# Kernel tuning notes

Measured on AMD Instinct MI355X. Metric: run time of the kernel, lower is better.

The kernel has to match this reference:

```python
import jax, jax.numpy as jnp
import numpy as np

DIM = 256          # model dim
H = 8              # num heads
E = DIM // H       # head dim = 32
M = 32             # ball size
NB = 8192          # number of balls
N = NB * M         # total points = 262144
D3 = 3             # spatial dimensionality


def setup_inputs() -> dict:
    key = jax.random.key(0)
    ks = jax.random.split(key, 10)
    s = 1.0 / np.sqrt(DIM)
    return {
        "x": jax.random.normal(ks[0], (N, DIM), jnp.float32),
        "pos": jax.random.normal(ks[1], (N, D3), jnp.float32),
        "w_qkv": jax.random.normal(ks[2], (DIM, 3 * DIM), jnp.float32) * s,
        "b_qkv": jnp.zeros((3 * DIM,), jnp.float32),
        "w_pe": jax.random.normal(ks[3], (D3, DIM), jnp.float32) * (1.0 / np.sqrt(D3)),
        "b_pe": jnp.zeros((DIM,), jnp.float32),
        "w_proj": jax.random.normal(ks[4], (DIM, DIM), jnp.float32) * s,
        "b_proj": jnp.zeros((DIM,), jnp.float32),
        "sigma_att": -1.0 + 0.01 * jax.random.normal(ks[5], (1, H, 1, 1), jnp.float32),
    }


def reference(x, pos, w_qkv, b_qkv, w_pe, b_pe, w_proj, b_proj, sigma_att):
    n = x.shape[0] // M
    pos_b = pos.reshape(n, M, D3)                       # (n, m, 3)

    # eq. 9: relative position embedding wrt ball center
    centers = pos_b.mean(axis=1, keepdims=True)         # (n, 1, 3)
    rel = (pos_b - centers).reshape(n * M, D3)
    x = x + rel @ w_pe + b_pe                           # (N, DIM)

    # qkv projection; layout '(H E K)' with K fastest
    qkv = (x @ w_qkv + b_qkv).reshape(n, M, H, E, 3)
    q = jnp.transpose(qkv[..., 0], (0, 2, 1, 3))        # (n, H, m, E)
    k = jnp.transpose(qkv[..., 1], (0, 2, 1, 3))
    v = jnp.transpose(qkv[..., 2], (0, 2, 1, 3))

    # eq. 10: distance-based attention bias
    diff = pos_b[:, :, None, :] - pos_b[:, None, :, :]  # (n, m, m, 3)
    d2 = jnp.sum(diff * diff, axis=-1)
    dist = jnp.sqrt(jnp.maximum(d2, 1e-12))             # safe sqrt (grad at 0)
    bias = sigma_att * dist[:, None, :, :]              # (n, H, m, m)

    scale = 1.0 / np.sqrt(E)
    scores = jnp.einsum('nhme,nhke->nhmk', q, k) * scale + bias
    attn = jax.nn.softmax(scores, axis=-1)
    out = jnp.einsum('nhmk,nhke->nhme', attn, v)        # (n, H, m, E)
    out = jnp.transpose(out, (0, 2, 1, 3)).reshape(n * M, DIM)
    return out @ w_proj + b_proj
```

## Files before the change

### kernel.cpp

```cpp
#include <hip/hip_runtime.h>

#define NPTS   262144
#define NBALLS 8192
#define MSZ    32

typedef unsigned short u16;
typedef __attribute__((ext_vector_type(8))) unsigned short u16x8;
typedef __attribute__((ext_vector_type(4))) unsigned short u16x4;
typedef __attribute__((ext_vector_type(8))) __bf16 bf16x8;
typedef __attribute__((ext_vector_type(4))) float f32x4;
typedef __attribute__((ext_vector_type(2))) unsigned u32x2;

__device__ inline u16 f2bf(float f) {
    unsigned u = __builtin_bit_cast(unsigned, f);
    u += 0x7fffu + ((u >> 16) & 1u);
    return (u16)(u >> 16);
}

__device__ inline unsigned pk2(float lo, float hi) {
    return (unsigned)f2bf(lo) | ((unsigned)f2bf(hi) << 16);
}

__device__ inline f32x4 mfma16(u16x8 a, u16x8 b, f32x4 c) {
    return __builtin_amdgcn_mfma_f32_16x16x32_bf16(
        __builtin_bit_cast(bf16x8, a), __builtin_bit_cast(bf16x8, b), c, 0, 0, 0);
}

__device__ inline void gload_lds16(const u16* g, u16* l) {
    __builtin_amdgcn_global_load_lds(
        (const __attribute__((address_space(1))) void*)g,
        (__attribute__((address_space(3))) void*)l, 16, 0, 0);
}

__global__ __launch_bounds__(256) void k0_wprep(const float* __restrict__ w_qkv,
                                                const float* __restrict__ b_qkv,
                                                const float* __restrict__ w_proj,
                                                u16* __restrict__ wqkvT,
                                                u16* __restrict__ wpF,
                                                float* __restrict__ bq) {
    int idx = blockIdx.x * 256 + threadIdx.x;
    if (idx < 768 * 256) {
        int cp = idx >> 8, r = idx & 255;
        int k = cp >> 8, rem = cp & 255, h = rem >> 5, e = rem & 31;
        int orig = h * 96 + e * 3 + k;
        wqkvT[cp * 256 + r] = f2bf(w_qkv[r * 768 + orig]);
        if (r == 0) bq[cp] = b_qkv[orig];
    } else {
        int tid2 = idx - 768 * 256;
        int lane = tid2 & 63, ch = tid2 >> 6;
        int hk = ch & 7, gct = ch >> 3;
        int r15 = lane & 15, g4 = lane >> 4;
        u16x8 o;
#pragma unroll
        for (int j = 0; j < 8; ++j)
            o[j] = f2bf(w_proj[(size_t)(hk * 32 + g4 * 8 + j) * 256 + gct * 16 + r15]);
        *(u16x8*)&wpF[(size_t)tid2 * 8] = o;
    }
}

__global__ __launch_bounds__(512, 4) void k1_qkv(const float* __restrict__ x,
                                                 const float* __restrict__ pos,
                                                 const float* __restrict__ w_pe,
                                                 const float* __restrict__ b_pe,
                                                 const u16* __restrict__ wqkvT,
                                                 const float* __restrict__ bq,
                                                 u16* __restrict__ qkv2) {
    __shared__ __align__(16) u16 Astage[128 * 64];
    __shared__ __align__(16) u16 Bs[2][128 * 64];
    __shared__ float ps_s[384];
    __shared__ float ctr_s[4][3];
    __shared__ float rel_s[128][3];
    __shared__ float wpe_s[3][256];
    __shared__ float bpe_s[256];

    int id = blockIdx.x;
    int rt = (id >> 3) + (id & 7) * 256;
    int t = threadIdx.x;
    int lane = t & 63, wv = t >> 6;
    int r15 = lane & 15, g4 = lane >> 4;
    int wr = wv >> 1, wc = wv & 1;
    int rowbase = rt * 128;

    if (t < 384) ps_s[t] = pos[(size_t)rt * 384 + t];
    if (t < 256) bpe_s[t] = b_pe[t];
    for (int i = t; i < 768; i += 512) ((float*)wpe_s)[i] = w_pe[i];
    __syncthreads();
    if (t < 12) {
        int b = t / 3, m = t % 3;
        float s = 0.f;
#pragma unroll
        for (int j = 0; j < MSZ; ++j) s += ps_s[(b * 32 + j) * 3 + m];
        ctr_s[b][m] = s * (1.0f / MSZ);
    }
    __syncthreads();
    if (t < 384) {
        int p = t / 3, m = t % 3;
        ((float*)rel_s)[t] = ps_s[t] - ctr_s[p >> 5][m];
    }
#pragma unroll
    for (int i = 0; i < 2; ++i) {
        int c = i * 512 + t;
        int row = c >> 3, sg = c & 7;
        gload_lds16(&wqkvT[(size_t)row * 256 + (sg ^ (row & 7)) * 8], &Bs[0][c * 8]);
    }
    __syncthreads();

    u16x8 af[2][8];
#pragma unroll
    for (int kt = 0; kt < 4; ++kt) {
#pragma unroll
        for (int i = 0; i < 2; ++i) {
            int c = i * 512 + t;
            int row = c >> 3, g = c & 7;
            int kk0 = kt * 64 + g * 8;
            float4 xa = *(const float4*)&x[(size_t)(rowbase + row) * 256 + kk0];
            float4 xb = *(const float4*)&x[(size_t)(rowbase + row) * 256 + kk0 + 4];
            float r0 = rel_s[row][0], r1 = rel_s[row][1], r2 = rel_s[row][2];
            u16x8 o;
#pragma unroll
            for (int m = 0; m < 8; ++m) {
                float xv = (m < 4) ? ((const float*)&xa)[m] : ((const float*)&xb)[m - 4];
                float v = fmaf(r0, wpe_s[0][kk0 + m],
                          fmaf(r1, wpe_s[1][kk0 + m],
                          fmaf(r2, wpe_s[2][kk0 + m], xv))) + bpe_s[kk0 + m];
                o[m] = f2bf(v);
            }
            *(u16x8*)&Astage[(row * 8 + (g ^ (row & 7))) * 8] = o;
        }
        __syncthreads();
#pragma unroll
        for (int ks = 0; ks < 2; ++ks)
#pragma unroll
            for (int i = 0; i < 2; ++i) {
                int R = wr * 32 + i * 16 + r15;
                af[i][2 * kt + ks] =
                    *(const u16x8*)&Astage[R * 64 + (((ks * 4 + g4) ^ (R & 7)) * 8)];
            }
        __syncthreads();
    }

    f32x4 acc[4][2];
#pragma unroll
    for (int j = 0; j < 4; ++j)
#pragma unroll
        for (int i = 0; i < 2; ++i) acc[j][i] = (f32x4){0.f, 0.f, 0.f, 0.f};

    const int ball = rt * 4 + wr;
    for (int ct = 0; ct < 6; ++ct) {
#pragma unroll
        for (int kt = 0; kt < 4; ++kt) {
            int cur = kt & 1;
            if (kt < 3 || ct < 5) {
                int nct = (kt < 3) ? ct : ct + 1;
                int nkt = (kt < 3) ? kt + 1 : 0;
#pragma unroll
                for (int i = 0; i < 2; ++i) {
                    int c = i * 512 + t;
                    int row = c >> 3, sg = c & 7;
                    gload_lds16(&wqkvT[(size_t)(nct * 128 + row) * 256 + nkt * 64 + (sg ^ (row & 7)) * 8],
                                &Bs[cur ^ 1][c * 8]);
                }
            }
#pragma unroll
            for (int ks = 0; ks < 2; ++ks) {
                u16x8 b[4];
#pragma unroll
                for (int j = 0; j < 4; ++j) {
                    int C = wc * 64 + j * 16 + r15;
                    b[j] = *(const u16x8*)&Bs[cur][C * 64 + (((ks * 4 + g4) ^ (C & 7)) * 8)];
                }
#pragma unroll
                for (int j = 0; j < 4; ++j)
#pragma unroll
                    for (int i = 0; i < 2; ++i)
                        acc[j][i] = mfma16(b[j], af[i][2 * kt + ks], acc[j][i]);
            }
            if (kt == 3) {
#pragma unroll
                for (int j = 0; j < 4; ++j) {
                    int cp0 = ct * 128 + wc * 64 + j * 16 + g4 * 4;
                    float4 bias = *(const float4*)&bq[cp0];
                    int mat = cp0 >> 8, rem = cp0 & 255, h = rem >> 5, e0 = rem & 31;
                    size_t base = (size_t)ball * 24576 + mat * 8192 + h * 1024 + e0;
#pragma unroll
                    for (int i = 0; i < 2; ++i) {
                        int point = i * 16 + r15;
                        unsigned lo = pk2(acc[j][i][0] + bias.x, acc[j][i][1] + bias.y);
                        unsigned hi = pk2(acc[j][i][2] + bias.z, acc[j][i][3] + bias.w);
                        *(u32x2*)&qkv2[base + point * 32] = (u32x2){lo, hi};
                        acc[j][i] = (f32x4){0.f, 0.f, 0.f, 0.f};
                    }
                }
            }
            __syncthreads();
        }
    }
}

__global__ __launch_bounds__(256) void k23_attnproj(const float* __restrict__ pos,
                                                    const float* __restrict__ sigma,
                                                    const u16* __restrict__ qkv2,
                                                    const u16* __restrict__ wpF,
                                                    const float* __restrict__ bp,
                                                    float* __restrict__ out) {
    int ball = blockIdx.x, t = threadIdx.x;
    __shared__ float ps[MSZ][3];
    __shared__ float dist_s[MSZ][33];
    __shared__ __align__(16) u16 V_s[MSZ][256];
    __shared__ __align__(16) u16 P_s[4][MSZ][40];
    __shared__ __align__(16) u16 ao_s[MSZ][264];

    const size_t ballbase = (size_t)ball * 24576;

    if (t < MSZ * 3) ((float*)ps)[t] = pos[(size_t)ball * (MSZ * 3) + t];
    __syncthreads();
    for (int p = t; p < 1024; p += 256) {
        int m = p >> 5, k = p & 31;
        float dx = ps[m][0] - ps[k][0], dy = ps[m][1] - ps[k][1], dz = ps[m][2] - ps[k][2];
        dist_s[m][k] = sqrtf(fmaxf(dx * dx + dy * dy + dz * dz, 1e-12f));
    }
#pragma unroll
    for (int i = 0; i < 4; ++i) {
        int c = i * 256 + t;
        int h = c >> 7, wi = c & 127;
        int point = wi >> 2, g4w = wi & 3;
        int col8 = h * 32 + g4w * 8;
        int cs = col8 ^ (((point >> 3) & 3) << 4);
        *(u16x8*)&V_s[point][cs] = *(const u16x8*)&qkv2[ballbase + 16384 + (size_t)c * 8];
    }
    __syncthreads();

    int lane = t & 63, wv = t >> 6;
    int r15 = lane & 15, g4 = lane >> 4;
    const float scale = 0.17677669529663687f;

#pragma unroll
    for (int hh = 0; hh < 2; ++hh) {
        int h = wv * 2 + hh;
        float sig = sigma[h];
        u16x8 aq[2], bk[2];
#pragma unroll
        for (int i = 0; i < 2; ++i) {
            aq[i] = *(const u16x8*)&qkv2[ballbase + h * 1024 + (size_t)(i * 16 + r15) * 32 + g4 * 8];
            bk[i] = *(const u16x8*)&qkv2[ballbase + 8192 + h * 1024 + (size_t)(i * 16 + r15) * 32 + g4 * 8];
        }
        f32x4 s[2][2];
#pragma unroll
        for (int i = 0; i < 2; ++i)
#pragma unroll
            for (int j = 0; j < 2; ++j) s[i][j] = (f32x4){0.f, 0.f, 0.f, 0.f};
#pragma unroll
        for (int i = 0; i < 2; ++i)
#pragma unroll
            for (int j = 0; j < 2; ++j)
                s[i][j] = mfma16(aq[i], bk[j], s[i][j]);

#pragma unroll
        for (int i = 0; i < 2; ++i) {
#pragma unroll
            for (int r = 0; r < 4; ++r) {
                int row = i * 16 + g4 * 4 + r;
                float v0 = s[i][0][r] * scale + sig * dist_s[row][r15];
                float v1 = s[i][1][r] * scale + sig * dist_s[row][16 + r15];
                float m = fmaxf(v0, v1);
                m = fmaxf(m, __shfl_xor(m, 1));
                m = fmaxf(m, __shfl_xor(m, 2));
                m = fmaxf(m, __shfl_xor(m, 4));
                m = fmaxf(m, __shfl_xor(m, 8));
                float e0 = __expf(v0 - m), e1 = __expf(v1 - m);
                float su = e0 + e1;
                su += __shfl_xor(su, 1);
                su += __shfl_xor(su, 2);
                su += __shfl_xor(su, 4);
                su += __shfl_xor(su, 8);
                float rin = 1.0f / su;
                P_s[wv][row][r15]      = f2bf(e0 * rin);
                P_s[wv][row][16 + r15] = f2bf(e1 * rin);
            }
        }
        u16x8 pa[2];
#pragma unroll
        for (int i = 0; i < 2; ++i)
            pa[i] = *(const u16x8*)&P_s[wv][i * 16 + r15][g4 * 8];
        u16x8 bv[2];
#pragma unroll
        for (int j = 0; j < 2; ++j) {
#pragma unroll
            for (int jj = 0; jj < 8; ++jj) {
                int kp = g4 * 8 + jj;
                int colv = h * 32 + j * 16 + r15;
                bv[j][jj] = V_s[kp][colv ^ (((kp >> 3) & 3) << 4)];
            }
        }
        f32x4 o[2][2];
#pragma unroll
        for (int i = 0; i < 2; ++i)
#pragma unroll
            for (int j = 0; j < 2; ++j) o[i][j] = (f32x4){0.f, 0.f, 0.f, 0.f};
#pragma unroll
        for (int i = 0; i < 2; ++i)
#pragma unroll
            for (int j = 0; j < 2; ++j)
                o[i][j] = mfma16(pa[i], bv[j], o[i][j]);
#pragma unroll
        for (int i = 0; i < 2; ++i)
#pragma unroll
            for (int j = 0; j < 2; ++j)
#pragma unroll
                for (int r = 0; r < 4; ++r) {
                    int row = i * 16 + g4 * 4 + r;
                    int col = h * 32 + j * 16 + r15;
                    ao_s[row][col] = f2bf(o[i][j][r]);
                }
    }
    __syncthreads();

    f32x4 pacc[4][2];
#pragma unroll
    for (int tt = 0; tt < 4; ++tt)
#pragma unroll
        for (int i = 0; i < 2; ++i) pacc[tt][i] = (f32x4){0.f, 0.f, 0.f, 0.f};
#pragma unroll
    for (int hk = 0; hk < 8; ++hk) {
        u16x8 apj[2];
#pragma unroll
        for (int i = 0; i < 2; ++i)
            apj[i] = *(const u16x8*)&ao_s[i * 16 + r15][hk * 32 + g4 * 8];
#pragma unroll
        for (int tt = 0; tt < 4; ++tt) {
            int gct = wv * 4 + tt;
            u16x8 b = *(const u16x8*)&wpF[(size_t)((gct * 8 + hk) * 64 + lane) * 8];
            pacc[tt][0] = mfma16(apj[0], b, pacc[tt][0]);
            pacc[tt][1] = mfma16(apj[1], b, pacc[tt][1]);
        }
    }
#pragma unroll
    for (int tt = 0; tt < 4; ++tt) {
        int ct = (wv * 4 + tt) * 16;
        float bb = bp[ct + r15];
#pragma unroll
        for (int i = 0; i < 2; ++i)
#pragma unroll
            for (int r = 0; r < 4; ++r) {
                int row = ball * MSZ + i * 16 + g4 * 4 + r;
                out[(size_t)row * 256 + ct + r15] = pacc[tt][i][r] + bb;
            }
    }
}

extern "C" void kernel_launch(void* const* d_in, const int* in_sizes, int n_in,
                              void* d_out, int out_size, void* d_ws, size_t ws_size,
                              hipStream_t stream) {
    (void)in_sizes; (void)n_in; (void)out_size; (void)ws_size;
    const float* x      = (const float*)d_in[0];
    const float* pos    = (const float*)d_in[1];
    const float* w_qkv  = (const float*)d_in[2];
    const float* b_qkv  = (const float*)d_in[3];
    const float* w_pe   = (const float*)d_in[4];
    const float* b_pe   = (const float*)d_in[5];
    const float* w_proj = (const float*)d_in[6];
    const float* b_proj = (const float*)d_in[7];
    const float* sigma  = (const float*)d_in[8];
    float* out = (float*)d_out;

    u16* qkv2   = (u16*)d_ws;
    u16* wqkvT  = qkv2 + (size_t)NPTS * 768;
    u16* wpF    = wqkvT + 768 * 256;
    float* bq   = (float*)(wpF + 65536);

    k0_wprep<<<800, 256, 0, stream>>>(w_qkv, b_qkv, w_proj, wqkvT, wpF, bq);
    k1_qkv<<<2048, 512, 0, stream>>>(x, pos, w_pe, b_pe, wqkvT, bq, qkv2);
    k23_attnproj<<<NBALLS, 256, 0, stream>>>(pos, sigma, qkv2, wpF, b_proj, out);
}
```

Before: 431.8 us.

## Load QKV weights directly from global in MFMA fragment order, drop LDS staging

The weight-prep kernel now writes w_qkv as bf16 already arranged in per-lane MFMA fragment order. The QKV GEMM kernel then reads B fragments straight from global/L2 with coalesced 16-byte loads. This removes the double-buffered LDS staging, the async global-to-LDS copies and the per-k-tile barriers. The cost is that every wave re-reads the weights from cache without sharing through LDS, so the kernel depends more on L2 bandwidth and load latency.

```diff
diff --git a/kernel.cpp b/kernel.cpp
--- a/kernel.cpp
+++ b/kernel.cpp
@@ -26,27 +26,32 @@
         __builtin_bit_cast(bf16x8, a), __builtin_bit_cast(bf16x8, b), c, 0, 0, 0);
 }
 
-__device__ inline void gload_lds16(const u16* g, u16* l) {
-    __builtin_amdgcn_global_load_lds(
-        (const __attribute__((address_space(1))) void*)g,
-        (__attribute__((address_space(3))) void*)l, 16, 0, 0);
-}
-
 __global__ __launch_bounds__(256) void k0_wprep(const float* __restrict__ w_qkv,
                                                 const float* __restrict__ b_qkv,
                                                 const float* __restrict__ w_proj,
-                                                u16* __restrict__ wqkvT,
+                                                u16* __restrict__ wqkvF,
                                                 u16* __restrict__ wpF,
                                                 float* __restrict__ bq) {
-    int idx = blockIdx.x * 256 + threadIdx.x;
-    if (idx < 768 * 256) {
-        int cp = idx >> 8, r = idx & 255;
-        int k = cp >> 8, rem = cp & 255, h = rem >> 5, e = rem & 31;
-        int orig = h * 96 + e * 3 + k;
-        wqkvT[cp * 256 + r] = f2bf(w_qkv[r * 768 + orig]);
-        if (r == 0) bq[cp] = b_qkv[orig];
+    int g = blockIdx.x * 256 + threadIdx.x;
+    if (g < 768) {
+        int cp = g;
+        int mat = cp >> 8, rem = cp & 255, h = rem >> 5, e = rem & 31;
+        bq[cp] = b_qkv[h * 96 + e * 3 + mat];
+    }
+    if (g < 24576) {
+        int lane = g & 63, ks = (g >> 6) & 7, tile = g >> 9;
+        int r15 = lane & 15, g4 = lane >> 4;
+        int cp = tile * 16 + r15;
+        int mat = cp >> 8, rem = cp & 255, h = rem >> 5, e = rem & 31;
+        int orig = h * 96 + e * 3 + mat;
+        int k0 = ks * 32 + g4 * 8;
+        u16x8 o;
+#pragma unroll
+        for (int j = 0; j < 8; ++j)
+            o[j] = f2bf(w_qkv[(size_t)(k0 + j) * 768 + orig]);
+        *(u16x8*)&wqkvF[(size_t)g * 8] = o;
     } else {
-        int tid2 = idx - 768 * 256;
+        int tid2 = g - 24576;
         int lane = tid2 & 63, ch = tid2 >> 6;
         int hk = ch & 7, gct = ch >> 3;
         int r15 = lane & 15, g4 = lane >> 4;
@@ -62,11 +67,10 @@
                                                  const float* __restrict__ pos,
                                                  const float* __restrict__ w_pe,
                                                  const float* __restrict__ b_pe,
-                                                 const u16* __restrict__ wqkvT,
+                                                 const u16* __restrict__ wqkvF,
                                                  const float* __restrict__ bq,
                                                  u16* __restrict__ qkv2) {
     __shared__ __align__(16) u16 Astage[128 * 64];
-    __shared__ __align__(16) u16 Bs[2][128 * 64];
     __shared__ float ps_s[384];
     __shared__ float ctr_s[4][3];
     __shared__ float rel_s[128][3];
@@ -96,12 +100,6 @@
     if (t < 384) {
         int p = t / 3, m = t % 3;
         ((float*)rel_s)[t] = ps_s[t] - ctr_s[p >> 5][m];
-    }
-#pragma unroll
-    for (int i = 0; i < 2; ++i) {
-        int c = i * 512 + t;
-        int row = c >> 3, sg = c & 7;
-        gload_lds16(&wqkvT[(size_t)row * 256 + (sg ^ (row & 7)) * 8], &Bs[0][c * 8]);
     }
     __syncthreads();
 
@@ -146,53 +144,36 @@
         for (int i = 0; i < 2; ++i) acc[j][i] = (f32x4){0.f, 0.f, 0.f, 0.f};
 
     const int ball = rt * 4 + wr;
+#pragma unroll
     for (int ct = 0; ct < 6; ++ct) {
 #pragma unroll
-        for (int kt = 0; kt < 4; ++kt) {
-            int cur = kt & 1;
-            if (kt < 3 || ct < 5) {
-                int nct = (kt < 3) ? ct : ct + 1;
-                int nkt = (kt < 3) ? kt + 1 : 0;
-#pragma unroll
-                for (int i = 0; i < 2; ++i) {
-                    int c = i * 512 + t;
-                    int row = c >> 3, sg = c & 7;
-                    gload_lds16(&wqkvT[(size_t)(nct * 128 + row) * 256 + nkt * 64 + (sg ^ (row & 7)) * 8],
-                                &Bs[cur ^ 1][c * 8]);
-                }
-            }
-#pragma unroll
-            for (int ks = 0; ks < 2; ++ks) {
-                u16x8 b[4];
-#pragma unroll
-                for (int j = 0; j < 4; ++j) {
-                    int C = wc * 64 + j * 16 + r15;
-                    b[j] = *(const u16x8*)&Bs[cur][C * 64 + (((ks * 4 + g4) ^ (C & 7)) * 8)];
-                }
-#pragma unroll
-                for (int j = 0; j < 4; ++j)
-#pragma unroll
-                    for (int i = 0; i < 2; ++i)
-                        acc[j][i] = mfma16(b[j], af[i][2 * kt + ks], acc[j][i]);
-            }
-            if (kt == 3) {
-#pragma unroll
-                for (int j = 0; j < 4; ++j) {
-                    int cp0 = ct * 128 + wc * 64 + j * 16 + g4 * 4;
-                    float4 bias = *(const float4*)&bq[cp0];
-                    int mat = cp0 >> 8, rem = cp0 & 255, h = rem >> 5, e0 = rem & 31;
-                    size_t base = (size_t)ball * 24576 + mat * 8192 + h * 1024 + e0;
-#pragma unroll
-                    for (int i = 0; i < 2; ++i) {
-                        int point = i * 16 + r15;
-                        unsigned lo = pk2(acc[j][i][0] + bias.x, acc[j][i][1] + bias.y);
-                        unsigned hi = pk2(acc[j][i][2] + bias.z, acc[j][i][3] + bias.w);
-                        *(u32x2*)&qkv2[base + point * 32] = (u32x2){lo, hi};
-                        acc[j][i] = (f32x4){0.f, 0.f, 0.f, 0.f};
-                    }
-                }
-            }
-            __syncthreads();
+        for (int ks = 0; ks < 8; ++ks) {
+            u16x8 b[4];
+#pragma unroll
+            for (int j = 0; j < 4; ++j) {
+                int tile = ct * 8 + wc * 4 + j;
+                b[j] = *(const u16x8*)&wqkvF[(size_t)((tile * 8 + ks) * 64 + lane) * 8];
+            }
+#pragma unroll
+            for (int j = 0; j < 4; ++j)
+#pragma unroll
+                for (int i = 0; i < 2; ++i)
+                    acc[j][i] = mfma16(b[j], af[i][ks], acc[j][i]);
+        }
+#pragma unroll
+        for (int j = 0; j < 4; ++j) {
+            int cp0 = ct * 128 + wc * 64 + j * 16 + g4 * 4;
+            float4 bias = *(const float4*)&bq[cp0];
+            int mat = cp0 >> 8, rem = cp0 & 255, h = rem >> 5, e0 = rem & 31;
+            size_t base = (size_t)ball * 24576 + mat * 8192 + h * 1024 + e0;
+#pragma unroll
+            for (int i = 0; i < 2; ++i) {
+                int point = i * 16 + r15;
+                unsigned lo = pk2(acc[j][i][0] + bias.x, acc[j][i][1] + bias.y);
+                unsigned hi = pk2(acc[j][i][2] + bias.z, acc[j][i][3] + bias.w);
+                *(u32x2*)&qkv2[base + point * 32] = (u32x2){lo, hi};
+                acc[j][i] = (f32x4){0.f, 0.f, 0.f, 0.f};
+            }
         }
     }
 }
@@ -364,11 +345,11 @@
     float* out = (float*)d_out;
 
     u16* qkv2   = (u16*)d_ws;
-    u16* wqkvT  = qkv2 + (size_t)NPTS * 768;
-    u16* wpF    = wqkvT + 768 * 256;
+    u16* wqkvF  = qkv2 + (size_t)NPTS * 768;
+    u16* wpF    = wqkvF + 196608;
     float* bq   = (float*)(wpF + 65536);
 
-    k0_wprep<<<800, 256, 0, stream>>>(w_qkv, b_qkv, w_proj, wqkvT, wpF, bq);
-    k1_qkv<<<2048, 512, 0, stream>>>(x, pos, w_pe, b_pe, wqkvT, bq, qkv2);
+    k0_wprep<<<128, 256, 0, stream>>>(w_qkv, b_qkv, w_proj, wqkvF, wpF, bq);
+    k1_qkv<<<2048, 512, 0, stream>>>(x, pos, w_pe, b_pe, wqkvF, bq, qkv2);
     k23_attnproj<<<NBALLS, 256, 0, stream>>>(pos, sigma, qkv2, wpF, b_proj, out);
 }
```

New measurement: 546.1 us. 1.26x slower.

## Halve QKV block tile to 64 rows and load A fragments directly from global

Applied to the files above, without the earlier changes.

The QKV projection kernel now uses 256-thread blocks covering 64 rows (two balls) instead of 512 threads covering 128 rows, and launches twice as many blocks. Each lane loads its own x values straight into MFMA A-fragment registers, which removes the LDS staging buffer and its barriers. The weight prefetch is also moved ahead of the centroid computation and the ct loop is unrolled. The trade-off is that every block reloads the full weight matrix for half as many rows, doubling weight traffic through LDS, and the per-lane global loads of x are less coalesced.

```diff
diff --git a/kernel.cpp b/kernel.cpp
--- a/kernel.cpp
+++ b/kernel.cpp
@@ -58,34 +58,39 @@
     }
 }
 
-__global__ __launch_bounds__(512, 4) void k1_qkv(const float* __restrict__ x,
+__global__ __launch_bounds__(256, 4) void k1_qkv(const float* __restrict__ x,
                                                  const float* __restrict__ pos,
                                                  const float* __restrict__ w_pe,
                                                  const float* __restrict__ b_pe,
                                                  const u16* __restrict__ wqkvT,
                                                  const float* __restrict__ bq,
                                                  u16* __restrict__ qkv2) {
-    __shared__ __align__(16) u16 Astage[128 * 64];
     __shared__ __align__(16) u16 Bs[2][128 * 64];
-    __shared__ float ps_s[384];
-    __shared__ float ctr_s[4][3];
-    __shared__ float rel_s[128][3];
+    __shared__ float ps_s[192];
+    __shared__ float ctr_s[2][3];
+    __shared__ float rel_s[64][3];
     __shared__ float wpe_s[3][256];
     __shared__ float bpe_s[256];
 
     int id = blockIdx.x;
-    int rt = (id >> 3) + (id & 7) * 256;
+    int rt = (id >> 3) + (id & 7) * 512;
     int t = threadIdx.x;
     int lane = t & 63, wv = t >> 6;
     int r15 = lane & 15, g4 = lane >> 4;
     int wr = wv >> 1, wc = wv & 1;
-    int rowbase = rt * 128;
-
-    if (t < 384) ps_s[t] = pos[(size_t)rt * 384 + t];
-    if (t < 256) bpe_s[t] = b_pe[t];
-    for (int i = t; i < 768; i += 512) ((float*)wpe_s)[i] = w_pe[i];
-    __syncthreads();
-    if (t < 12) {
+    int rowbase = rt * 64;
+
+    if (t < 192) ps_s[t] = pos[(size_t)rt * 192 + t];
+    bpe_s[t] = b_pe[t];
+    for (int i = t; i < 768; i += 256) ((float*)wpe_s)[i] = w_pe[i];
+#pragma unroll
+    for (int i = 0; i < 4; ++i) {
+        int c = i * 256 + t;
+        int row = c >> 3, sg = c & 7;
+        gload_lds16(&wqkvT[(size_t)row * 256 + (sg ^ (row & 7)) * 8], &Bs[0][c * 8]);
+    }
+    __syncthreads();
+    if (t < 6) {
         int b = t / 3, m = t % 3;
         float s = 0.f;
 #pragma unroll
@@ -93,50 +98,34 @@
         ctr_s[b][m] = s * (1.0f / MSZ);
     }
     __syncthreads();
-    if (t < 384) {
+    if (t < 192) {
         int p = t / 3, m = t % 3;
         ((float*)rel_s)[t] = ps_s[t] - ctr_s[p >> 5][m];
     }
+    __syncthreads();
+
+    u16x8 af[2][8];
 #pragma unroll
     for (int i = 0; i < 2; ++i) {
-        int c = i * 512 + t;
-        int row = c >> 3, sg = c & 7;
-        gload_lds16(&wqkvT[(size_t)row * 256 + (sg ^ (row & 7)) * 8], &Bs[0][c * 8]);
-    }
-    __syncthreads();
-
-    u16x8 af[2][8];
-#pragma unroll
-    for (int kt = 0; kt < 4; ++kt) {
-#pragma unroll
-        for (int i = 0; i < 2; ++i) {
-            int c = i * 512 + t;
-            int row = c >> 3, g = c & 7;
-            int kk0 = kt * 64 + g * 8;
-            float4 xa = *(const float4*)&x[(size_t)(rowbase + row) * 256 + kk0];
-            float4 xb = *(const float4*)&x[(size_t)(rowbase + row) * 256 + kk0 + 4];
-            float r0 = rel_s[row][0], r1 = rel_s[row][1], r2 = rel_s[row][2];
+        int lrow = wr * 32 + i * 16 + r15;
+        size_t xbase = (size_t)(rowbase + lrow) * 256;
+        float r0 = rel_s[lrow][0], r1 = rel_s[lrow][1], r2 = rel_s[lrow][2];
+#pragma unroll
+        for (int ks = 0; ks < 8; ++ks) {
+            int k0 = ks * 32 + g4 * 8;
+            float4 xa = *(const float4*)&x[xbase + k0];
+            float4 xb = *(const float4*)&x[xbase + k0 + 4];
             u16x8 o;
 #pragma unroll
             for (int m = 0; m < 8; ++m) {
                 float xv = (m < 4) ? ((const float*)&xa)[m] : ((const float*)&xb)[m - 4];
-                float v = fmaf(r0, wpe_s[0][kk0 + m],
-                          fmaf(r1, wpe_s[1][kk0 + m],
-                          fmaf(r2, wpe_s[2][kk0 + m], xv))) + bpe_s[kk0 + m];
+                float v = fmaf(r0, wpe_s[0][k0 + m],
+                          fmaf(r1, wpe_s[1][k0 + m],
+                          fmaf(r2, wpe_s[2][k0 + m], xv))) + bpe_s[k0 + m];
                 o[m] = f2bf(v);
             }
-            *(u16x8*)&Astage[(row * 8 + (g ^ (row & 7))) * 8] = o;
-        }
-        __syncthreads();
-#pragma unroll
-        for (int ks = 0; ks < 2; ++ks)
-#pragma unroll
-            for (int i = 0; i < 2; ++i) {
-                int R = wr * 32 + i * 16 + r15;
-                af[i][2 * kt + ks] =
-                    *(const u16x8*)&Astage[R * 64 + (((ks * 4 + g4) ^ (R & 7)) * 8)];
-            }
-        __syncthreads();
+            af[i][ks] = o;
+        }
     }
 
     f32x4 acc[4][2];
@@ -145,17 +134,18 @@
 #pragma unroll
         for (int i = 0; i < 2; ++i) acc[j][i] = (f32x4){0.f, 0.f, 0.f, 0.f};
 
-    const int ball = rt * 4 + wr;
+    const int ball = rt * 2 + wr;
+#pragma unroll
     for (int ct = 0; ct < 6; ++ct) {
 #pragma unroll
         for (int kt = 0; kt < 4; ++kt) {
             int cur = kt & 1;
-            if (kt < 3 || ct < 5) {
-                int nct = (kt < 3) ? ct : ct + 1;
-                int nkt = (kt < 3) ? kt + 1 : 0;
-#pragma unroll
-                for (int i = 0; i < 2; ++i) {
-                    int c = i * 512 + t;
+            int it = ct * 4 + kt;
+            if (it < 23) {
+                int nit = it + 1, nct = nit >> 2, nkt = nit & 3;
+#pragma unroll
+                for (int i = 0; i < 4; ++i) {
+                    int c = i * 256 + t;
                     int row = c >> 3, sg = c & 7;
                     gload_lds16(&wqkvT[(size_t)(nct * 128 + row) * 256 + nkt * 64 + (sg ^ (row & 7)) * 8],
                                 &Bs[cur ^ 1][c * 8]);
@@ -369,6 +359,6 @@
     float* bq   = (float*)(wpF + 65536);
 
     k0_wprep<<<800, 256, 0, stream>>>(w_qkv, b_qkv, w_proj, wqkvT, wpF, bq);
-    k1_qkv<<<2048, 512, 0, stream>>>(x, pos, w_pe, b_pe, wqkvT, bq, qkv2);
+    k1_qkv<<<4096, 256, 0, stream>>>(x, pos, w_pe, b_pe, wqkvT, bq, qkv2);
     k23_attnproj<<<NBALLS, 256, 0, stream>>>(pos, sigma, qkv2, wpF, b_proj, out);
 }
```

After: 798.4 us. 1.85x slower.
